# Performance work log

Measured on AMD Instinct MI355X. Metric: run time of the kernel, lower is better.

The kernel has to match this reference:

```python
import jax, jax.numpy as jnp
import numpy as np

EPS = 1e-6

def _conv(x, w, padding):
    # x: [B,C,H,W], w: [O,I,kh,kw]
    return jax.lax.conv_general_dilated(x, w, window_strides=(1, 1), padding=padding,
                                        dimension_numbers=('NCHW', 'OIHW', 'NCHW'))

def setup_inputs() -> dict:
    key = jax.random.key(0)
    ks = jax.random.split(key, 8)
    C = 512
    B, H, W = 4, 64, 64
    s1 = 1.0 / np.sqrt(C)          # 1x1 conv fan-in
    s3 = 1.0 / np.sqrt(C * 9)      # 3x3 conv fan-in
    return {
        'x': jax.random.normal(ks[0], (B, C, H, W), dtype=jnp.float32),
        'ln_w': jnp.ones((C,), dtype=jnp.float32),
        'ln_b': jnp.zeros((C,), dtype=jnp.float32),
        'wq': jax.random.normal(ks[1], (C, C, 1, 1), dtype=jnp.float32) * s1,
        'wk': jax.random.normal(ks[2], (C, C, 3, 3), dtype=jnp.float32) * s3,
        'wv': jax.random.normal(ks[3], (C, C, 3, 3), dtype=jnp.float32) * s3,
        'wp': jax.random.normal(ks[4], (C, C, 1, 1), dtype=jnp.float32) * s1,
        'bp': jnp.zeros((C,), dtype=jnp.float32),
    }

def reference(x, ln_w, ln_b, wq, wk, wv, wp, bp):
    # channels_first LayerNorm over C
    u = jnp.mean(x, axis=1, keepdims=True)
    s = jnp.mean((x - u) ** 2, axis=1, keepdims=True)
    h = (x - u) / jnp.sqrt(s + EPS)
    h = ln_w[None, :, None, None] * h + ln_b[None, :, None, None]

    q = _conv(h, wq, 'VALID')           # 1x1
    k = _conv(h, wk, [(1, 1), (1, 1)])  # 3x3, pad 1
    v = _conv(h, wv, [(1, 1), (1, 1)])

    b, c, H, W = q.shape
    hw = H * W
    q = q.reshape(b, c, hw)
    k = k.reshape(b, c, hw)
    v = v.reshape(b, c, hw)

    scale = jnp.asarray(int(c) ** (-0.5), q.dtype)
    attn = jnp.einsum('bcm,bcn->bmn', q, k) * scale  # [b, hw_q, hw_k]
    attn = jax.nn.softmax(attn, axis=2)
    out = jnp.einsum('bcn,bmn->bcm', v, attn)        # [b, c, hw_q]
    out = out.reshape(b, c, H, W)

    out = _conv(out, wp, 'VALID') + bp[None, :, None, None]
    return x + out
```

## Files before the change

kernel.cpp:

```cpp
#include <hip/hip_runtime.h>
#include <hip/hip_bf16.h>

#define C_DIM 512
#define HW    4096
#define BATCH 4
#define PW    66
#define PPIX  (PW*PW)

typedef __attribute__((ext_vector_type(8))) short bf16x8;
typedef __attribute__((ext_vector_type(4))) float f32x4;
typedef __attribute__((ext_vector_type(16))) float f32x16;
typedef __attribute__((ext_vector_type(2))) long long l64x2;

static __device__ __forceinline__ short f2b(float f) {
    union { float f; unsigned u; } v; v.f = f;
    unsigned r = v.u + 0x7fffu + ((v.u >> 16) & 1u);
    return (short)(r >> 16);
}
static __device__ __forceinline__ float b2f(short s) {
    union { unsigned u; float f; } v; v.u = ((unsigned)(unsigned short)s) << 16;
    return v.f;
}

static __device__ __forceinline__ f32x4 zero4() {
    f32x4 v = {0.f, 0.f, 0.f, 0.f};
    return v;
}
static __device__ __forceinline__ f32x16 zero16() {
    f32x16 v = {0.f,0.f,0.f,0.f, 0.f,0.f,0.f,0.f, 0.f,0.f,0.f,0.f, 0.f,0.f,0.f,0.f};
    return v;
}

static __device__ __forceinline__ void gload16(const void* g, void* l) {
    __builtin_amdgcn_global_load_lds(
        (__attribute__((address_space(1))) void*)g,
        (__attribute__((address_space(3))) void*)l, 16, 0, 0);
}

__global__ void k_cvt_bf16(const float* __restrict__ in, short* __restrict__ out, int n) {
    int i = blockIdx.x * 256 + threadIdx.x;
    if (i < n) out[i] = f2b(in[i]);
}

__global__ void k_reorder_w38(const float* __restrict__ w, unsigned char* __restrict__ out) {
    int i = blockIdx.x * 256 + threadIdx.x;
    int o = i / 576;
    int p8 = (i - o * 576) * 8;
    int kc2 = p8 >> 6;
    int tap = kc2 >> 3;
    int p = p8 & 63;
    int g = (p >> 4) & 3, half = (p >> 3) & 1;
    int c0 = (kc2 & 7) * 64 + half * 32 + g * 8;
    const float* src = w + ((size_t)o * 512 + c0) * 9 + tap;
    float f0 = src[0] * 64.f, f1 = src[9] * 64.f, f2 = src[18] * 64.f, f3 = src[27] * 64.f;
    float f4 = src[36] * 64.f, f5 = src[45] * 64.f, f6 = src[54] * 64.f, f7 = src[63] * 64.f;
    int lo = __builtin_amdgcn_cvt_pk_fp8_f32(f0, f1, 0, false);
    lo     = __builtin_amdgcn_cvt_pk_fp8_f32(f2, f3, lo, true);
    int hi = __builtin_amdgcn_cvt_pk_fp8_f32(f4, f5, 0, false);
    hi     = __builtin_amdgcn_cvt_pk_fp8_f32(f6, f7, hi, true);
    *(uint2*)&out[(size_t)o * 4608 + p8] = make_uint2((unsigned)lo, (unsigned)hi);
}

__global__ void k_cvt_k8(const short* __restrict__ in, unsigned char* __restrict__ out) {
    int i = blockIdx.x * 256 + threadIdx.x;
    int m = i >> 6;
    int p = (i & 63) * 8;
    int kcp = p >> 6, g = (p >> 4) & 3, half = (p >> 3) & 1;
    int chb = (kcp * 2 + half) * 32 + g * 8;
    bf16x8 v = *(const bf16x8*)&in[(size_t)m * 512 + chb];
    int lo = __builtin_amdgcn_cvt_pk_fp8_f32(b2f(v[0]), b2f(v[1]), 0, false);
    lo     = __builtin_amdgcn_cvt_pk_fp8_f32(b2f(v[2]), b2f(v[3]), lo, true);
    int hi = __builtin_amdgcn_cvt_pk_fp8_f32(b2f(v[4]), b2f(v[5]), 0, false);
    hi     = __builtin_amdgcn_cvt_pk_fp8_f32(b2f(v[6]), b2f(v[7]), hi, true);
    *(uint2*)&out[(size_t)m * 512 + p] = make_uint2((unsigned)lo, (unsigned)hi);
}

__global__ void k_ln_fused(const float* __restrict__ x, const float* __restrict__ lnw,
                           const float* __restrict__ lnb, short* __restrict__ hp,
                           unsigned char* __restrict__ hp8) {
    __shared__ float red[8][64];
    __shared__ float mean_s[64], rstd_s[64];
    __shared__ short tile[64][65];
    int bid = blockIdx.x;
    int y = bid & 63, b = bid >> 6;
    int t = threadIdx.x;
    int px = t & 63, cg = t >> 6;
    const float* xb = x + (size_t)b * C_DIM * HW + (size_t)y * 64;

    float s = 0.f, sq = 0.f;
    for (int c = cg * 128; c < cg * 128 + 128; ++c) {
        float v = xb[(size_t)c * HW + px];
        s += v; sq += v * v;
    }
    red[cg][px] = s;
    red[4 + cg][px] = sq;
    __syncthreads();
    if (t < 64) {
        float S = red[0][t] + red[1][t] + red[2][t] + red[3][t];
        float Q = red[4][t] + red[5][t] + red[6][t] + red[7][t];
        float mu  = S * (1.0f / C_DIM);
        float var = Q * (1.0f / C_DIM) - mu * mu;
        mean_s[t] = mu;
        rstd_s[t] = 1.0f / sqrtf(var + 1e-6f);
    }
    __syncthreads();
    float mu = mean_s[px], rs = rstd_s[px];
    int cj = t & 63, pj = t >> 6;
    int chn = t & 7, pxe = t >> 3;
    int clocal = (chn & 1) * 32 + ((chn >> 1) & 3) * 8;
    for (int ct = 0; ct < 8; ++ct) {
        int c0 = ct * 64;
        #pragma unroll
        for (int cc = 0; cc < 64; cc += 4) {
            int c = c0 + cc + cg;
            float v = xb[(size_t)c * HW + px];
            tile[cc + cg][px] = f2b((v - mu) * rs * lnw[c] + lnb[c]);
        }
        __syncthreads();
        #pragma unroll
        for (int pp = 0; pp < 64; pp += 4) {
            int pidx = pp + pj;
            size_t dst = ((size_t)b * PPIX + (size_t)(y + 1) * PW + 1 + pidx) * C_DIM + c0 + cj;
            hp[dst] = tile[cj][pidx];
        }
        #pragma unroll
        for (int h = 0; h < 2; ++h) {
            int pix = pxe + h * 32;
            float f0 = b2f(tile[clocal + 0][pix]);
            float f1 = b2f(tile[clocal + 1][pix]);
            float f2 = b2f(tile[clocal + 2][pix]);
            float f3 = b2f(tile[clocal + 3][pix]);
            float f4 = b2f(tile[clocal + 4][pix]);
            float f5 = b2f(tile[clocal + 5][pix]);
            float f6 = b2f(tile[clocal + 6][pix]);
            float f7 = b2f(tile[clocal + 7][pix]);
            int lo = __builtin_amdgcn_cvt_pk_fp8_f32(f0, f1, 0, false);
            lo     = __builtin_amdgcn_cvt_pk_fp8_f32(f2, f3, lo, true);
            int hi = __builtin_amdgcn_cvt_pk_fp8_f32(f4, f5, 0, false);
            hi     = __builtin_amdgcn_cvt_pk_fp8_f32(f6, f7, hi, true);
            size_t row = (size_t)b * PPIX + (size_t)(y + 1) * PW + 1 + pix;
            *(uint2*)&hp8[row * 512 + c0 + chn * 8] = make_uint2((unsigned)lo, (unsigned)hi);
        }
        __syncthreads();
    }
}

template<int TAPS, int GMODE, int EPI>
__global__ __launch_bounds__(256, 2) void k_gemm(
        const short* __restrict__ A, const short* __restrict__ Bw,
        void* __restrict__ Out, const float* __restrict__ bias,
        const float* __restrict__ resid)
{
    constexpr int K = TAPS * 512;
    constexpr int NKC = K / 64;
    __shared__ short Alds[128 * 64];
    __shared__ short Blds[128 * 64];
    int bid = blockIdx.x;
    int mt = bid & 31, nt = (bid >> 5) & 3, b = bid >> 7;
    int m0 = mt * 128, n0 = nt * 128;
    int t = threadIdx.x;
    int lane = t & 63, w = t >> 6;
    int wm = w >> 1, wn = w & 1;
    int g = lane >> 4, li = lane & 15;
    int srow = t >> 3, schunk = t & 7;
    const short* Ab = A + (GMODE == 0 ? (size_t)b * PPIX * C_DIM : (size_t)b * HW * C_DIM);

    f32x4 acc[4][4];
    #pragma unroll
    for (int i = 0; i < 4; ++i)
        #pragma unroll
        for (int j = 0; j < 4; ++j) acc[i][j] = zero4();

    for (int kc = 0; kc < NKC; ++kc) {
        int tap = (TAPS == 9) ? (kc >> 3) : 4;
        int cb  = (kc & 7) * 64;
        __syncthreads();
        #pragma unroll
        for (int r = 0; r < 4; ++r) {
            int row = r * 32 + srow;
            size_t goff;
            if (GMODE == 0) {
                int m = m0 + row;
                int yy = m >> 6, xx = m & 63;
                int pp = (yy + tap / 3) * PW + xx + (tap % 3);
                goff = (size_t)pp * C_DIM + cb + schunk * 8;
            } else {
                goff = (size_t)(m0 + row) * K + kc * 64 + schunk * 8;
            }
            gload16(Ab + goff, Alds + row * 64 + schunk * 8);
        }
        #pragma unroll
        for (int r = 0; r < 4; ++r) {
            int row = r * 32 + srow;
            size_t goff = (size_t)(n0 + row) * K + kc * 64 + schunk * 8;
            gload16(Bw + goff, Blds + row * 64 + schunk * 8);
        }
        __syncthreads();
        #pragma unroll
        for (int ks = 0; ks < 2; ++ks) {
            int koff = ks * 32 + g * 8;
            bf16x8 af[4], bfr[4];
            #pragma unroll
            for (int i = 0; i < 4; ++i)
                af[i] = *(const bf16x8*)&Alds[(wm * 64 + i * 16 + li) * 64 + koff];
            #pragma unroll
            for (int j = 0; j < 4; ++j)
                bfr[j] = *(const bf16x8*)&Blds[(wn * 64 + j * 16 + li) * 64 + koff];
            #pragma unroll
            for (int i = 0; i < 4; ++i)
                #pragma unroll
                for (int j = 0; j < 4; ++j)
                    acc[i][j] = __builtin_amdgcn_mfma_f32_16x16x32_bf16(af[i], bfr[j], acc[i][j], 0, 0, 0);
        }
    }
    #pragma unroll
    for (int fm = 0; fm < 4; ++fm) {
        #pragma unroll
        for (int fn = 0; fn < 4; ++fn) {
            int mrow = m0 + wm * 64 + fm * 16 + g * 4;
            int ncol = n0 + wn * 64 + fn * 16 + li;
            if constexpr (EPI == 0) {
                #pragma unroll
                for (int i = 0; i < 4; ++i) {
                    size_t dst = ((size_t)b * HW + mrow + i) * C_DIM + ncol;
                    ((short*)Out)[dst] = f2b(acc[fm][fn][i]);
                }
            } else if constexpr (EPI == 1) {
                size_t dst = ((size_t)b * C_DIM + ncol) * HW + mrow;
                short4 sv = make_short4(f2b(acc[fm][fn][0]), f2b(acc[fm][fn][1]),
                                        f2b(acc[fm][fn][2]), f2b(acc[fm][fn][3]));
                *(short4*)((short*)Out + dst) = sv;
            } else {
                size_t dst = ((size_t)b * C_DIM + ncol) * HW + mrow;
                float bb = bias[ncol];
                float4 xr = *(const float4*)(resid + dst);
                float4 o;
                o.x = acc[fm][fn][0] + bb + xr.x;
                o.y = acc[fm][fn][1] + bb + xr.y;
                o.z = acc[fm][fn][2] + bb + xr.z;
                o.w = acc[fm][fn][3] + bb + xr.w;
                *(float4*)((float*)Out + dst) = o;
            }
        }
    }
}

__global__ __launch_bounds__(256, 2) void k_gemm_kv8(
        const unsigned char* __restrict__ A8, const unsigned char* __restrict__ Bk8,
        const unsigned char* __restrict__ Bv8, short* __restrict__ OutK,
        short* __restrict__ OutV)
{
    __shared__ unsigned char Alds[2][10240];
    __shared__ unsigned char Bklds[2][10240];
    __shared__ unsigned char Bvlds[2][10240];
    int bid = blockIdx.x;
    int mt = bid & 31, nt = (bid >> 5) & 3, b = bid >> 7;
    int m0 = mt * 128, n0 = nt * 128;
    int t = threadIdx.x;
    int lane = t & 63, w = t >> 6;
    int wm = w >> 1, wn = w & 1;
    int g = lane >> 4, li = lane & 15;
    const unsigned char* Ab = A8 + (size_t)b * PPIX * 512;

    int srowv[3], schv[3];
    #pragma unroll
    for (int r = 0; r < 3; ++r) {
        int slot = r * 256 + t;
        int row = slot / 5;
        int ch = slot - row * 5;
        srowv[r] = row;
        schv[r] = (ch < 4) ? ch * 16 : 0;
    }
    bool act2 = (w < 2);

    f32x4 accK[4][4], accV[4][4];
    #pragma unroll
    for (int i = 0; i < 4; ++i)
        #pragma unroll
        for (int j = 0; j < 4; ++j) { accK[i][j] = zero4(); accV[i][j] = zero4(); }

    auto STAGE = [&](int bf, int kc2) {
        int tap = kc2 >> 3;
        int gofs = (kc2 & 7) * 64;
        int ty3 = tap / 3, tx3 = tap % 3;
        #pragma unroll
        for (int r = 0; r < 3; ++r) {
            if (r < 2 || act2) {
                int row = srowv[r];
                int m = m0 + row;
                int yy = m >> 6, xx = m & 63;
                int pp = (yy + ty3) * PW + xx + tx3;
                int dst = (r * 256 + t) * 16;
                gload16(Ab + (size_t)pp * 512 + gofs + schv[r], &Alds[bf][dst]);
                size_t gb = (size_t)(n0 + row) * 4608 + kc2 * 64 + schv[r];
                gload16(Bk8 + gb, &Bklds[bf][dst]);
                gload16(Bv8 + gb, &Bvlds[bf][dst]);
            }
        }
    };

    auto COMPUTE = [&](int bf) {
        l64x2 av[4], bk[4], bv[4];
        #pragma unroll
        for (int i = 0; i < 4; ++i)
            av[i] = *(const l64x2*)&Alds[bf][(wm * 64 + i * 16 + li) * 80 + g * 16];
        #pragma unroll
        for (int j = 0; j < 4; ++j)
            bk[j] = *(const l64x2*)&Bklds[bf][(wn * 64 + j * 16 + li) * 80 + g * 16];
        #pragma unroll
        for (int j = 0; j < 4; ++j)
            bv[j] = *(const l64x2*)&Bvlds[bf][(wn * 64 + j * 16 + li) * 80 + g * 16];
        #pragma unroll
        for (int h = 0; h < 2; ++h) {
            #pragma unroll
            for (int i = 0; i < 4; ++i)
                #pragma unroll
                for (int j = 0; j < 4; ++j)
                    accK[i][j] = __builtin_amdgcn_mfma_f32_16x16x32_fp8_fp8(
                        av[i][h], bk[j][h], accK[i][j], 0, 0, 0);
            #pragma unroll
            for (int i = 0; i < 4; ++i)
                #pragma unroll
                for (int j = 0; j < 4; ++j)
                    accV[i][j] = __builtin_amdgcn_mfma_f32_16x16x32_fp8_fp8(
                        av[i][h], bv[j][h], accV[i][j], 0, 0, 0);
        }
    };

    STAGE(0, 0);
    __syncthreads();
    int bf = 0;
    for (int kc2 = 0; kc2 < 72; ++kc2) {
        if (kc2 + 1 < 72) STAGE(bf ^ 1, kc2 + 1);
        COMPUTE(bf);
        __syncthreads();
        bf ^= 1;
    }

    const float SCL = 0.015625f;
    #pragma unroll
    for (int fm = 0; fm < 4; ++fm) {
        #pragma unroll
        for (int fn = 0; fn < 4; ++fn) {
            int mrow = m0 + wm * 64 + fm * 16 + g * 4;
            int ncol = n0 + wn * 64 + fn * 16 + li;
            #pragma unroll
            for (int i = 0; i < 4; ++i) {
                size_t dst = ((size_t)b * HW + mrow + i) * C_DIM + ncol;
                OutK[dst] = f2b(accK[fm][fn][i] * SCL);
            }
            size_t dstv = ((size_t)b * C_DIM + ncol) * HW + mrow;
            short4 sv = make_short4(f2b(accV[fm][fn][0] * SCL), f2b(accV[fm][fn][1] * SCL),
                                    f2b(accV[fm][fn][2] * SCL), f2b(accV[fm][fn][3] * SCL));
            *(short4*)(OutV + dstv) = sv;
        }
    }
}

#define KT 32
#define NTILES 64
__global__ __launch_bounds__(512, 2) void k_attn(
        const short* __restrict__ qT, const unsigned char* __restrict__ kT8,
        const short* __restrict__ vg, short* __restrict__ O0,
        short* __restrict__ O1, float* __restrict__ L0, float* __restrict__ L1)
{
    __shared__ __align__(16) short pool[73728];
    unsigned char* Kp8 = (unsigned char*)pool;
    short* Vp = pool + 16384;
    short* Pp = pool + 57344;

    int bid0 = blockIdx.x;
    int bid = (bid0 & 7) * 32 + (bid0 >> 3);
    int qt = bid & 31, ks = (bid >> 5) & 1, b = bid >> 6;
    int m0 = qt * 128;
    int t = threadIdx.x, lane = t & 63, w = t >> 6;
    int g = lane >> 4, li = lane & 15;
    int l31 = lane & 31, l5 = lane >> 5;

    const unsigned char* kb8 = kT8 + ((size_t)b * HW + (size_t)ks * 2048) * 512;
    const short* vb = vg + (size_t)b * C_DIM * HW + ks * 2048;

    long long qf8[16];
    {
        const short* qrow = qT + ((size_t)b * HW + m0 + w * 16 + li) * C_DIM;
        #pragma unroll
        for (int kc = 0; kc < 16; ++kc) {
            bf16x8 qv = *(const bf16x8*)&qrow[kc * 32 + g * 8];
            int lo = __builtin_amdgcn_cvt_pk_fp8_f32(b2f(qv[0]), b2f(qv[1]), 0, false);
            lo     = __builtin_amdgcn_cvt_pk_fp8_f32(b2f(qv[2]), b2f(qv[3]), lo, true);
            int hi = __builtin_amdgcn_cvt_pk_fp8_f32(b2f(qv[4]), b2f(qv[5]), 0, false);
            hi     = __builtin_amdgcn_cvt_pk_fp8_f32(b2f(qv[6]), b2f(qv[7]), hi, true);
            qf8[kc] = ((long long)(unsigned)hi << 32) | (unsigned)lo;
        }
    }
    f32x16 oacc[8];
    #pragma unroll
    for (int a = 0; a < 8; ++a) oacc[a] = zero16();
    float lsum = 0.f;

    const unsigned char* ksrc8 = kb8 + (size_t)(t & 31) * 512 + (t >> 5) * 16;
    int voff[5];
    #pragma unroll
    for (int r = 0; r < 5; ++r) {
        int D = r * 512 + t;
        int ch = D / 5;
        int c  = D - ch * 5;
        voff[r] = (c < 4) ? ch * 4096 + c * 8 : 0;
    }

    const float SC = 0.044194173824159216f * 1.4426950408889634f;

    auto STAGE = [&](int buf, int nt) {
        int n0 = nt * KT;
        const unsigned char* kS = ksrc8 + (size_t)n0 * 512;
        unsigned char* kD = Kp8 + buf * 16384 + t * 16;
        gload16(kS, kD);
        gload16(kS + 256, kD + 8192);
        short* vD = Vp + buf * 20480 + t * 8;
        #pragma unroll
        for (int r = 0; r < 5; ++r)
            gload16(vb + voff[r] + n0, vD + r * 4096);
    };

    STAGE(0, 0);
    asm volatile("s_waitcnt vmcnt(0)" ::: "memory");
    __builtin_amdgcn_s_barrier();
    __builtin_amdgcn_sched_barrier(0);

    int buf = 0;
    for (int nt = 0; nt < NTILES; ++nt) {
        if (nt + 1 < NTILES) STAGE(buf ^ 1, nt + 1);

        const unsigned char* kbase8 = Kp8 + buf * 16384 + g * 512 + li * 16;
        f32x4 s0[2], s1[2];
        s0[0] = zero4(); s0[1] = zero4(); s1[0] = zero4(); s1[1] = zero4();
        __builtin_amdgcn_s_setprio(1);
        #pragma unroll
        for (int kcp = 0; kcp < 8; ++kcp) {
            #pragma unroll
            for (int fn = 0; fn < 2; ++fn) {
                l64x2 kv = *(const l64x2*)&kbase8[kcp * 2048 + fn * 256];
                s0[fn] = __builtin_amdgcn_mfma_f32_16x16x32_fp8_fp8(kv[0], qf8[2 * kcp],     s0[fn], 0, 0, 0);
                s1[fn] = __builtin_amdgcn_mfma_f32_16x16x32_fp8_fp8(kv[1], qf8[2 * kcp + 1], s1[fn], 0, 0, 0);
            }
        }
        __builtin_amdgcn_s_setprio(0);
        #pragma unroll
        for (int fn = 0; fn < 2; ++fn) {
            float e0 = exp2f((s0[fn][0] + s1[fn][0]) * SC);
            float e1 = exp2f((s0[fn][1] + s1[fn][1]) * SC);
            float e2 = exp2f((s0[fn][2] + s1[fn][2]) * SC);
            float e3 = exp2f((s0[fn][3] + s1[fn][3]) * SC);
            lsum += (e0 + e1) + (e2 + e3);
            union { __hip_bfloat162 h; unsigned u; } p01, p23;
            p01.h = __float22bfloat162_rn(make_float2(e0, e1));
            p23.h = __float22bfloat162_rn(make_float2(e2, e3));
            *(uint2*)&Pp[(w * 16 + li) * 40 + fn * 16 + g * 4] = make_uint2(p01.u, p23.u);
        }

        asm volatile("s_waitcnt lgkmcnt(0)" ::: "memory");
        __builtin_amdgcn_s_barrier();
        __builtin_amdgcn_sched_barrier(0);

        const short* vbase = Vp + buf * 20480 + (size_t)w * 64 * 40;
        bf16x8 vf[2][2];
        #pragma unroll
        for (int cht = 0; cht < 2; ++cht)
            #pragma unroll
            for (int kx = 0; kx < 2; ++kx)
                vf[cht][kx] = *(const bf16x8*)&vbase[(cht * 32 + l31) * 40 + kx * 16 + l5 * 8];
        __builtin_amdgcn_s_setprio(1);
        #pragma unroll
        for (int q2 = 0; q2 < 4; ++q2) {
            #pragma unroll
            for (int kx = 0; kx < 2; ++kx) {
                bf16x8 pf = *(const bf16x8*)&Pp[(q2 * 32 + l31) * 40 + kx * 16 + l5 * 8];
                oacc[q2 * 2 + 0] = __builtin_amdgcn_mfma_f32_32x32x16_bf16(vf[0][kx], pf, oacc[q2 * 2 + 0], 0, 0, 0);
                oacc[q2 * 2 + 1] = __builtin_amdgcn_mfma_f32_32x32x16_bf16(vf[1][kx], pf, oacc[q2 * 2 + 1], 0, 0, 0);
            }
        }
        __builtin_amdgcn_s_setprio(0);

        asm volatile("s_waitcnt vmcnt(0)" ::: "memory");
        __builtin_amdgcn_s_barrier();
        __builtin_amdgcn_sched_barrier(0);
        buf ^= 1;
    }

    lsum += __shfl_xor(lsum, 16);
    lsum += __shfl_xor(lsum, 32);
    float* Lb = (ks ? L1 : L0) + (size_t)b * HW + m0 + w * 16;
    if (lane < 16) Lb[lane] = lsum;

    short* tp = pool + w * 9216;
    #pragma unroll
    for (int a = 0; a < 8; ++a) {
        int q2 = a >> 1, cht = a & 1;
        int q_l = q2 * 32 + l31;
        #pragma unroll
        for (int rq = 0; rq < 4; ++rq) {
            int chb = cht * 32 + rq * 8 + l5 * 4;
            union { __hip_bfloat162 h; unsigned u; } x01, x23;
            x01.h = __float22bfloat162_rn(make_float2(oacc[a][rq * 4 + 0], oacc[a][rq * 4 + 1]));
            x23.h = __float22bfloat162_rn(make_float2(oacc[a][rq * 4 + 2], oacc[a][rq * 4 + 3]));
            *(uint2*)&tp[q_l * 72 + chb] = make_uint2(x01.u, x23.u);
        }
    }
    asm volatile("s_waitcnt lgkmcnt(0)" ::: "memory");
    __builtin_amdgcn_sched_barrier(0);
    short* Ob = (ks ? O1 : O0) + ((size_t)b * HW + m0) * C_DIM + w * 64;
    #pragma unroll
    for (int qg = 0; qg < 16; ++qg) {
        int qr = qg * 8 + (lane >> 3);
        bf16x8 v = *(const bf16x8*)&tp[qr * 72 + (lane & 7) * 8];
        *(bf16x8*)&Ob[(size_t)qr * C_DIM + (lane & 7) * 8] = v;
    }
}

__global__ void k_att_comb(const short* __restrict__ O0, const short* __restrict__ O1,
                           const float* __restrict__ L0, const float* __restrict__ L1,
                           short* __restrict__ oatt) {
    int i = blockIdx.x * 256 + threadIdx.x;
    int row = i >> 6;
    int c0 = (i & 63) * 8;
    float r = 1.0f / (L0[row] + L1[row]);
    size_t base = (size_t)row * C_DIM + c0;
    bf16x8 a = *(const bf16x8*)&O0[base];
    bf16x8 c = *(const bf16x8*)&O1[base];
    bf16x8 o;
    #pragma unroll
    for (int j = 0; j < 8; ++j)
        o[j] = f2b((b2f(a[j]) + b2f(c[j])) * r);
    *(bf16x8*)&oatt[base] = o;
}

extern "C" void kernel_launch(void* const* d_in, const int* in_sizes, int n_in,
                              void* d_out, int out_size, void* d_ws, size_t ws_size,
                              hipStream_t stream) {
    const float* x    = (const float*)d_in[0];
    const float* ln_w = (const float*)d_in[1];
    const float* ln_b = (const float*)d_in[2];
    const float* wq   = (const float*)d_in[3];
    const float* wk   = (const float*)d_in[4];
    const float* wv   = (const float*)d_in[5];
    const float* wp   = (const float*)d_in[6];
    const float* bp   = (const float*)d_in[7];
    float* out = (float*)d_out;

    char* ws = (char*)d_ws;
    size_t off = 0;
    auto alloc = [&](size_t bytes) {
        char* p = ws + off;
        off += (bytes + 255) & ~(size_t)255;
        return p;
    };
    short* hp   = (short*)alloc((size_t)BATCH * PPIX * C_DIM * 2);
    unsigned char* hp8 = (unsigned char*)alloc((size_t)BATCH * PPIX * 512);
    short* wqb  = (short*)alloc((size_t)512 * 512 * 2);
    unsigned char* wk8 = (unsigned char*)alloc((size_t)512 * 4608);
    unsigned char* wv8 = (unsigned char*)alloc((size_t)512 * 4608);
    short* wpb  = (short*)alloc((size_t)512 * 512 * 2);
    short* qT   = (short*)alloc((size_t)BATCH * HW * C_DIM * 2);
    short* kT   = (short*)alloc((size_t)BATCH * HW * C_DIM * 2);
    short* vg   = (short*)alloc((size_t)BATCH * HW * C_DIM * 2);
    short* oatt = (short*)alloc((size_t)BATCH * HW * C_DIM * 2);
    float* mean = (float*)alloc((size_t)BATCH * HW * 4);
    float* rstd = (float*)alloc((size_t)BATCH * HW * 4);

    hipMemsetAsync(hp, 0, (size_t)BATCH * PPIX * C_DIM * 2, stream);
    hipMemsetAsync(hp8, 0, (size_t)BATCH * PPIX * 512, stream);
    k_cvt_bf16<<<1024, 256, 0, stream>>>(wq, wqb, 512 * 512);
    k_cvt_bf16<<<1024, 256, 0, stream>>>(wp, wpb, 512 * 512);
    k_reorder_w38<<<1152, 256, 0, stream>>>(wk, wk8);
    k_reorder_w38<<<1152, 256, 0, stream>>>(wv, wv8);
    k_ln_fused<<<256, 256, 0, stream>>>(x, ln_w, ln_b, hp, hp8);

    k_gemm<1, 0, 0><<<512, 256, 0, stream>>>(hp, wqb, qT, nullptr, nullptr);
    k_gemm_kv8<<<512, 256, 0, stream>>>(hp8, wk8, wv8, kT, vg);

    unsigned char* kT8 = hp8;
    k_cvt_k8<<<4096, 256, 0, stream>>>(kT, kT8);

    short* Op0 = hp;
    short* Op1 = oatt;
    float* Ls0 = mean;
    float* Ls1 = rstd;
    k_attn<<<256, 512, 0, stream>>>(qT, kT8, vg, Op0, Op1, Ls0, Ls1);
    k_att_comb<<<4096, 256, 0, stream>>>(Op0, Op1, Ls0, Ls1, oatt);

    k_gemm<1, 1, 2><<<512, 256, 0, stream>>>(oatt, wpb, out, bp, x);
}
```

Before: 340.2 us.

## Compute Q projection in FP8 and drop the bf16 normalized activation buffer

Replaces the bf16 1x1 Q-projection GEMM with a new FP8 MFMA GEMM that reads the existing FP8 padded LayerNorm output and an FP8-reordered Wq. This removes the bf16 padded activation writes in the LayerNorm kernel, its memset, and the bf16 Wq conversion, which cuts memory traffic and halves GEMM operand bytes. The cost is lower precision for Q, since the query projection now uses e4m3 inputs, which may affect attention accuracy.

```diff
diff --git a/kernel.cpp b/kernel.cpp
--- a/kernel.cpp
+++ b/kernel.cpp
@@ -61,6 +61,22 @@
     *(uint2*)&out[(size_t)o * 4608 + p8] = make_uint2((unsigned)lo, (unsigned)hi);
 }
 
+__global__ void k_reorder_w18(const float* __restrict__ w, unsigned char* __restrict__ out) {
+    int i = blockIdx.x * 256 + threadIdx.x;
+    int o = i >> 6;
+    int p8 = (i & 63) * 8;
+    int grp = p8 >> 6;
+    int p = p8 & 63;
+    int g = (p >> 4) & 3, half = (p >> 3) & 1;
+    int c0 = grp * 64 + half * 32 + g * 8;
+    const float* src = w + (size_t)o * 512 + c0;
+    int lo = __builtin_amdgcn_cvt_pk_fp8_f32(src[0] * 64.f, src[1] * 64.f, 0, false);
+    lo     = __builtin_amdgcn_cvt_pk_fp8_f32(src[2] * 64.f, src[3] * 64.f, lo, true);
+    int hi = __builtin_amdgcn_cvt_pk_fp8_f32(src[4] * 64.f, src[5] * 64.f, 0, false);
+    hi     = __builtin_amdgcn_cvt_pk_fp8_f32(src[6] * 64.f, src[7] * 64.f, hi, true);
+    *(uint2*)&out[(size_t)o * 512 + p8] = make_uint2((unsigned)lo, (unsigned)hi);
+}
+
 __global__ void k_cvt_k8(const short* __restrict__ in, unsigned char* __restrict__ out) {
     int i = blockIdx.x * 256 + threadIdx.x;
     int m = i >> 6;
@@ -76,8 +92,7 @@
 }
 
 __global__ void k_ln_fused(const float* __restrict__ x, const float* __restrict__ lnw,
-                           const float* __restrict__ lnb, short* __restrict__ hp,
-                           unsigned char* __restrict__ hp8) {
+                           const float* __restrict__ lnb, unsigned char* __restrict__ hp8) {
     __shared__ float red[8][64];
     __shared__ float mean_s[64], rstd_s[64];
     __shared__ short tile[64][65];
@@ -105,7 +120,6 @@
     }
     __syncthreads();
     float mu = mean_s[px], rs = rstd_s[px];
-    int cj = t & 63, pj = t >> 6;
     int chn = t & 7, pxe = t >> 3;
     int clocal = (chn & 1) * 32 + ((chn >> 1) & 3) * 8;
     for (int ct = 0; ct < 8; ++ct) {
@@ -117,12 +131,6 @@
             tile[cc + cg][px] = f2b((v - mu) * rs * lnw[c] + lnb[c]);
         }
         __syncthreads();
-        #pragma unroll
-        for (int pp = 0; pp < 64; pp += 4) {
-            int pidx = pp + pj;
-            size_t dst = ((size_t)b * PPIX + (size_t)(y + 1) * PW + 1 + pidx) * C_DIM + c0 + cj;
-            hp[dst] = tile[cj][pidx];
-        }
         #pragma unroll
         for (int h = 0; h < 2; ++h) {
             int pix = pxe + h * 32;
@@ -357,6 +365,98 @@
     }
 }
 
+__global__ __launch_bounds__(256, 2) void k_gemm_q8(
+        const unsigned char* __restrict__ A8, const unsigned char* __restrict__ Bq8,
+        short* __restrict__ OutQ)
+{
+    __shared__ unsigned char Alds[2][10240];
+    __shared__ unsigned char Blds[2][10240];
+    int bid = blockIdx.x;
+    int mt = bid & 31, nt = (bid >> 5) & 3, b = bid >> 7;
+    int m0 = mt * 128, n0 = nt * 128;
+    int t = threadIdx.x;
+    int lane = t & 63, w = t >> 6;
+    int wm = w >> 1, wn = w & 1;
+    int g = lane >> 4, li = lane & 15;
+    const unsigned char* Ab = A8 + (size_t)b * PPIX * 512;
+
+    int srowv[3], schv[3];
+    #pragma unroll
+    for (int r = 0; r < 3; ++r) {
+        int slot = r * 256 + t;
+        int row = slot / 5;
+        int ch = slot - row * 5;
+        srowv[r] = row;
+        schv[r] = (ch < 4) ? ch * 16 : 0;
+    }
+    bool act2 = (w < 2);
+
+    f32x4 accQ[4][4];
+    #pragma unroll
+    for (int i = 0; i < 4; ++i)
+        #pragma unroll
+        for (int j = 0; j < 4; ++j) accQ[i][j] = zero4();
+
+    auto STAGE = [&](int bf, int kc2) {
+        int gofs = kc2 * 64;
+        #pragma unroll
+        for (int r = 0; r < 3; ++r) {
+            if (r < 2 || act2) {
+                int row = srowv[r];
+                int m = m0 + row;
+                int yy = m >> 6, xx = m & 63;
+                int pp = (yy + 1) * PW + xx + 1;
+                int dst = (r * 256 + t) * 16;
+                gload16(Ab + (size_t)pp * 512 + gofs + schv[r], &Alds[bf][dst]);
+                gload16(Bq8 + (size_t)(n0 + row) * 512 + gofs + schv[r], &Blds[bf][dst]);
+            }
+        }
+    };
+
+    auto COMPUTE = [&](int bf) {
+        l64x2 av[4], bq[4];
+        #pragma unroll
+        for (int i = 0; i < 4; ++i)
+            av[i] = *(const l64x2*)&Alds[bf][(wm * 64 + i * 16 + li) * 80 + g * 16];
+        #pragma unroll
+        for (int j = 0; j < 4; ++j)
+            bq[j] = *(const l64x2*)&Blds[bf][(wn * 64 + j * 16 + li) * 80 + g * 16];
+        #pragma unroll
+        for (int h = 0; h < 2; ++h)
+            #pragma unroll
+            for (int i = 0; i < 4; ++i)
+                #pragma unroll
+                for (int j = 0; j < 4; ++j)
+                    accQ[i][j] = __builtin_amdgcn_mfma_f32_16x16x32_fp8_fp8(
+                        av[i][h], bq[j][h], accQ[i][j], 0, 0, 0);
+    };
+
+    STAGE(0, 0);
+    __syncthreads();
+    int bf = 0;
+    for (int kc2 = 0; kc2 < 8; ++kc2) {
+        if (kc2 + 1 < 8) STAGE(bf ^ 1, kc2 + 1);
+        COMPUTE(bf);
+        __syncthreads();
+        bf ^= 1;
+    }
+
+    const float SCL = 0.015625f;
+    #pragma unroll
+    for (int fm = 0; fm < 4; ++fm) {
+        #pragma unroll
+        for (int fn = 0; fn < 4; ++fn) {
+            int mrow = m0 + wm * 64 + fm * 16 + g * 4;
+            int ncol = n0 + wn * 64 + fn * 16 + li;
+            #pragma unroll
+            for (int i = 0; i < 4; ++i) {
+                size_t dst = ((size_t)b * HW + mrow + i) * C_DIM + ncol;
+                OutQ[dst] = f2b(accQ[fm][fn][i] * SCL);
+            }
+        }
+    }
+}
+
 #define KT 32
 #define NTILES 64
 __global__ __launch_bounds__(512, 2) void k_attn(
@@ -556,7 +656,7 @@
     };
     short* hp   = (short*)alloc((size_t)BATCH * PPIX * C_DIM * 2);
     unsigned char* hp8 = (unsigned char*)alloc((size_t)BATCH * PPIX * 512);
-    short* wqb  = (short*)alloc((size_t)512 * 512 * 2);
+    unsigned char* wq8 = (unsigned char*)alloc((size_t)512 * 512);
     unsigned char* wk8 = (unsigned char*)alloc((size_t)512 * 4608);
     unsigned char* wv8 = (unsigned char*)alloc((size_t)512 * 4608);
     short* wpb  = (short*)alloc((size_t)512 * 512 * 2);
@@ -567,15 +667,14 @@
     float* mean = (float*)alloc((size_t)BATCH * HW * 4);
     float* rstd = (float*)alloc((size_t)BATCH * HW * 4);
 
-    hipMemsetAsync(hp, 0, (size_t)BATCH * PPIX * C_DIM * 2, stream);
     hipMemsetAsync(hp8, 0, (size_t)BATCH * PPIX * 512, stream);
-    k_cvt_bf16<<<1024, 256, 0, stream>>>(wq, wqb, 512 * 512);
     k_cvt_bf16<<<1024, 256, 0, stream>>>(wp, wpb, 512 * 512);
+    k_reorder_w18<<<128, 256, 0, stream>>>(wq, wq8);
     k_reorder_w38<<<1152, 256, 0, stream>>>(wk, wk8);
     k_reorder_w38<<<1152, 256, 0, stream>>>(wv, wv8);
-    k_ln_fused<<<256, 256, 0, stream>>>(x, ln_w, ln_b, hp, hp8);
-
-    k_gemm<1, 0, 0><<<512, 256, 0, stream>>>(hp, wqb, qT, nullptr, nullptr);
+    k_ln_fused<<<256, 256, 0, stream>>>(x, ln_w, ln_b, hp8);
+
+    k_gemm_q8<<<512, 256, 0, stream>>>(hp8, wq8, qT);
     k_gemm_kv8<<<512, 256, 0, stream>>>(hp8, wk8, wv8, kT, vg);
 
     unsigned char* kT8 = hp8;
```

New measurement: 327.1 us. 1.04x faster.
